# Optimization experiments

Hardware: AMD Instinct MI355X
Metric: run time of the kernel (lower is better)

The kernel has to match this reference:

```python
import jax, jax.numpy as jnp
import numpy as np

NUM_POINTS = 33  # must be 2n+1
N_T = 4_194_304  # number of time samples


def setup_inputs() -> dict:
    key = jax.random.key(0)
    k1, k2 = jax.random.split(key)
    x = jax.random.uniform(k1, (N_T,), dtype=jnp.float32)  # t in [0,1]
    P = jax.random.uniform(k2, (NUM_POINTS, 5), dtype=jnp.float32)
    P = (P - P.mean()) / P.std()  # mimics initLayers normalization
    return {"x": x, "P": P}


def _basis(d):
    """d: (N,1) -> quadratic Bezier basis (N,3) = [1, d, d^2] @ B."""
    B = jnp.array([[1., 0., 0.], [-2., 2., 0.], [1., -2., 1.]], dtype=d.dtype)
    tpow = jnp.concatenate([jnp.ones_like(d), d, d * d], axis=1)  # (N,3)
    return tpow @ B


def _forward(x, P):
    num_points = P.shape[0]
    S = num_points - 2  # num_splines
    p = P[:, :2]   # (num_points, 2) means
    s = P[:, 2:]   # (num_points, 3) packed symmetric 2x2: [a, b, c] -> [[a,b],[b,c]]
    # new_sigma_mat = sigma_mat^T @ sigma_mat (sigma_mat symmetric) packed back to 3 entries
    a, b, c = s[:, 0], s[:, 1], s[:, 2]
    sig = jnp.stack([a * a + b * b, b * (a + c), b * b + c * c], axis=1)  # (num_points, 3)

    t = x[:, None]                       # (N,1)
    N = x.shape[0]
    mu0 = jnp.zeros((N, 2), x.dtype)
    sg0 = jnp.zeros((N, 3), x.dtype)
    Pn0 = p[:3]                          # (3,2)
    Sn0 = sig[:3]                        # (3,3)
    ivals = jnp.arange(S - 1, dtype=x.dtype)
    Sm1 = jnp.asarray(S - 1, x.dtype)

    def step(carry, xs):
        Pn, Sn, mu, sg = carry
        i, p_next, s_next = xs
        d = (t * Sm1 - i) * 0.5                      # (N,1)
        choice = ((d >= 0) & (d <= 0.5)).astype(x.dtype)
        cw = jnp.cos(jnp.pi * d) ** 2
        sw = jnp.sin(jnp.pi * d) ** 2
        # mean control-point recurrence
        p0 = (Pn[0] + Pn[2]) / 4 + Pn[1] / 2
        p2 = p_next
        p1 = 2.0 * (Pn[2] - (p0 + p2) / 4)
        Pn2 = jnp.stack([p0, p1, p2])                # (3,2)
        f_prev = _basis(d + 0.5) @ Pn                # (N,2)
        f_curr = _basis(d) @ Pn2
        mu = (1 - choice) * mu + choice * (cw * f_prev + sw * f_curr)
        # variance control-point recurrence
        s0 = (Sn[0] + Sn[2]) / 16 + Sn[1] / 4
        s2 = s_next
        s1 = 4.0 * (Sn[2] - (s0 + s2) / 16)
        Sn2 = jnp.stack([s0, s1, s2])                # (3,3)
        g_prev = (_basis(d + 0.5) ** 2) @ Sn         # (N,3)
        g_curr = (_basis(d) ** 2) @ Sn2
        sg = (1 - choice) * sg + choice * (cw ** 2 * g_prev + sw ** 2 * g_curr)
        return (Pn2, Sn2, mu, sg), None

    (_, _, mu, sg), _ = jax.lax.scan(step, (Pn0, Sn0, mu0, sg0), (ivals, p[3:], sig[3:]))
    return mu, sg


def reference(x, P):
    return _forward(x, P)
```

## Files before the change

kernel.cpp:

```cpp
#include <hip/hip_runtime.h>
#include <math.h>

#define NENT 33
#define NQ   30
#define PPT  4
#define NBLK 2048

__device__ __forceinline__ unsigned short f2bf(float f) {
    unsigned int b = __float_as_uint(f);
    unsigned int r = (b + 0x7FFFu + ((b >> 16) & 1u)) >> 16;
    return (unsigned short)r;
}
__device__ __forceinline__ float bflo(unsigned int w) { return __uint_as_float(w << 16); }
__device__ __forceinline__ float bfhi(unsigned int w) { return __uint_as_float(w & 0xFFFF0000u); }

__global__ __launch_bounds__(256) void yuksel_fused(
    const float* __restrict__ x, const float* __restrict__ P,
    float* __restrict__ out, int N)
{
    __shared__ float stage[5][NENT];
    __shared__ uint2 qtab[5][NQ];
    const int tid = threadIdx.x;

    if (tid < NENT) {
        const int e = tid;
        float vals[5];
        if (e == 1) {
            float r0[5], r1[5], r2[5];
            for (int r = 0; r < 3; ++r) {
                float* dst = r==0 ? r0 : (r==1 ? r1 : r2);
                float a = P[r*5+2], b = P[r*5+3], c = P[r*5+4];
                dst[0] = P[r*5+0]; dst[1] = P[r*5+1];
                dst[2] = a*a + b*b; dst[3] = b*(a+c); dst[4] = b*b + c*c;
            }
            for (int k = 0; k < 2; ++k) vals[k] = (r0[k]+r2[k])*0.25f   + r1[k]*0.5f;
            for (int k = 2; k < 5; ++k) vals[k] = (r0[k]+r2[k])*0.0625f + r1[k]*0.25f;
        } else {
            float a = P[e*5+2], b = P[e*5+3], c = P[e*5+4];
            vals[0] = P[e*5+0]; vals[1] = P[e*5+1];
            vals[2] = a*a + b*b; vals[3] = b*(a+c); vals[4] = b*b + c*c;
        }
#pragma unroll
        for (int k = 0; k < 5; ++k) stage[k][e] = vals[k];
    }
    __syncthreads();

    if (tid < 5*NQ) {
        const int k = tid / NQ, e = tid % NQ;
        unsigned int h0 = f2bf(stage[k][e+0]), h1 = f2bf(stage[k][e+1]);
        unsigned int h2 = f2bf(stage[k][e+2]), h3 = f2bf(stage[k][e+3]);
        qtab[k][e] = make_uint2(h0 | (h1 << 16), h2 | (h3 << 16));
    }
    __syncthreads();

    const long long stride = (long long)gridDim.x * 256 * PPT;
    for (long long j0 = ((long long)blockIdx.x * 256 + tid) * PPT; j0 < N; j0 += stride) {
        float4 xv = *reinterpret_cast<const float4*>(x + j0);
        float xs[PPT] = { xv.x, xv.y, xv.z, xv.w };
        float mu[2*PPT], sg[3*PPT];

#pragma unroll
        for (int q = 0; q < PPT; ++q) {
            float u  = xs[q] * 30.0f;
            float fi = fminf(fmaxf(floorf(u), 0.0f), 29.0f);
            int   i  = (int)fi;
            float d  = (u - fi) * 0.5f;

            float cw  = 0.5f + 0.5f*__builtin_amdgcn_cosf(d);
            float sw  = 1.0f - cw;
            float cw2 = cw*cw, sw2 = sw*sw;

            float omd  = 1.0f - d;
            float om2d = 1.0f - 2.0f*d;
            float g    = d * om2d;
            float w0 = -cw * g;
            float w3 = -sw * g;
            float w1 = cw*(1.0f - 4.0f*d*d) + sw*omd*om2d;
            float w2 = cw*d*(1.0f + 2.0f*d) + 4.0f*sw*d*omd;

            float hp = 0.5f + d;
            float q14 = 1.0f - 4.0f*d*d;
            float v0 = -cw2 * g * (0.5f - d);
            float v3 = -sw2 * g * d;
            float v1 = cw2*q14*q14 + sw2*omd*omd*om2d;
            float v2 = cw2*2.0f*d*hp*hp + 16.0f*sw2*d*d*omd*omd;

            uint2 rpx = qtab[0][i];
            uint2 rpy = qtab[1][i];
            uint2 rs0 = qtab[2][i];
            uint2 rs1 = qtab[3][i];
            uint2 rs2 = qtab[4][i];

            mu[2*q+0] = w0*bflo(rpx.x) + w1*bfhi(rpx.x) + w2*bflo(rpx.y) + w3*bfhi(rpx.y);
            mu[2*q+1] = w0*bflo(rpy.x) + w1*bfhi(rpy.x) + w2*bflo(rpy.y) + w3*bfhi(rpy.y);
            sg[3*q+0] = v0*bflo(rs0.x) + v1*bfhi(rs0.x) + v2*bflo(rs0.y) + v3*bfhi(rs0.y);
            sg[3*q+1] = v0*bflo(rs1.x) + v1*bfhi(rs1.x) + v2*bflo(rs1.y) + v3*bfhi(rs1.y);
            sg[3*q+2] = v0*bflo(rs2.x) + v1*bfhi(rs2.x) + v2*bflo(rs2.y) + v3*bfhi(rs2.y);
        }

        float4* muOut = reinterpret_cast<float4*>(out + 2*j0);
        muOut[0] = make_float4(mu[0], mu[1], mu[2], mu[3]);
        muOut[1] = make_float4(mu[4], mu[5], mu[6], mu[7]);
        float4* sgOut = reinterpret_cast<float4*>(out + (size_t)2*N + 3*j0);
        sgOut[0] = make_float4(sg[0], sg[1], sg[2],  sg[3]);
        sgOut[1] = make_float4(sg[4], sg[5], sg[6],  sg[7]);
        sgOut[2] = make_float4(sg[8], sg[9], sg[10], sg[11]);
    }
}

extern "C" void kernel_launch(void* const* d_in, const int* in_sizes, int n_in,
                              void* d_out, int out_size, void* d_ws, size_t ws_size,
                              hipStream_t stream) {
    const float* x = (const float*)d_in[0];
    const float* P = (const float*)d_in[1];
    float* out = (float*)d_out;
    int N = in_sizes[0];

    const int threads = 256;
    const int per_block = threads * PPT;
    long long ntiles = (N + per_block - 1) / per_block;
    int blocks = (int)(ntiles < NBLK ? ntiles : NBLK);
    yuksel_fused<<<blocks, threads, 0, stream>>>(x, P, out, N);
}
```

Before: 26.38 us.

## Restructure per-wave chunking with LDS-staged coalesced sigma output stores

Each wave now processes a contiguous 256-element chunk, with every lane handling strided points. Loads and mu stores become lane-contiguous float2 writes, and the 3-wide sigma outputs are staged through LDS and written back as contiguous float4 stores. The intent is to replace the previous per-thread strided float4 writes with fully coalesced wave-wide stores. In exchange it adds LDS traffic, only a sched_barrier rather than a real wave-level sync around the LDS exchange, and a scalar tail path.

```diff
diff --git a/kernel.cpp b/kernel.cpp
--- a/kernel.cpp
+++ b/kernel.cpp
@@ -3,8 +3,9 @@
 
 #define NENT 33
 #define NQ   30
-#define PPT  4
 #define NBLK 2048
+#define WPB  4
+#define CHUNK 256
 
 __device__ __forceinline__ unsigned short f2bf(float f) {
     unsigned int b = __float_as_uint(f);
@@ -20,7 +21,10 @@
 {
     __shared__ float stage[5][NENT];
     __shared__ uint2 qtab[5][NQ];
-    const int tid = threadIdx.x;
+    __shared__ float sgbuf[WPB][3*CHUNK];
+    const int tid  = threadIdx.x;
+    const int lane = tid & 63;
+    const int wave = tid >> 6;
 
     if (tid < NENT) {
         const int e = tid;
@@ -53,14 +57,22 @@
     }
     __syncthreads();
 
-    const long long stride = (long long)gridDim.x * 256 * PPT;
-    for (long long j0 = ((long long)blockIdx.x * 256 + tid) * PPT; j0 < N; j0 += stride) {
-        float4 xv = *reinterpret_cast<const float4*>(x + j0);
-        float xs[PPT] = { xv.x, xv.y, xv.z, xv.w };
-        float mu[2*PPT], sg[3*PPT];
+    const int gwave = blockIdx.x * WPB + wave;
+    const long long chunk_stride = (long long)gridDim.x * WPB * CHUNK;
 
+    for (long long base = (long long)gwave * CHUNK; base < N; base += chunk_stride) {
+        const bool full = (base + CHUNK <= N);
+
+        float xs[4];
 #pragma unroll
-        for (int q = 0; q < PPT; ++q) {
+        for (int q = 0; q < 4; ++q) {
+            long long p = base + q*64 + lane;
+            xs[q] = (full || p < N) ? x[p] : 0.0f;
+        }
+
+        float m0[4], m1[4], sv0[4], sv1[4], sv2[4];
+#pragma unroll
+        for (int q = 0; q < 4; ++q) {
             float u  = xs[q] * 30.0f;
             float fi = fminf(fmaxf(floorf(u), 0.0f), 29.0f);
             int   i  = (int)fi;
@@ -78,7 +90,7 @@
             float w1 = cw*(1.0f - 4.0f*d*d) + sw*omd*om2d;
             float w2 = cw*d*(1.0f + 2.0f*d) + 4.0f*sw*d*omd;
 
-            float hp = 0.5f + d;
+            float hp  = 0.5f + d;
             float q14 = 1.0f - 4.0f*d*d;
             float v0 = -cw2 * g * (0.5f - d);
             float v3 = -sw2 * g * d;
@@ -91,20 +103,42 @@
             uint2 rs1 = qtab[3][i];
             uint2 rs2 = qtab[4][i];
 
-            mu[2*q+0] = w0*bflo(rpx.x) + w1*bfhi(rpx.x) + w2*bflo(rpx.y) + w3*bfhi(rpx.y);
-            mu[2*q+1] = w0*bflo(rpy.x) + w1*bfhi(rpy.x) + w2*bflo(rpy.y) + w3*bfhi(rpy.y);
-            sg[3*q+0] = v0*bflo(rs0.x) + v1*bfhi(rs0.x) + v2*bflo(rs0.y) + v3*bfhi(rs0.y);
-            sg[3*q+1] = v0*bflo(rs1.x) + v1*bfhi(rs1.x) + v2*bflo(rs1.y) + v3*bfhi(rs1.y);
-            sg[3*q+2] = v0*bflo(rs2.x) + v1*bfhi(rs2.x) + v2*bflo(rs2.y) + v3*bfhi(rs2.y);
+            m0[q]  = w0*bflo(rpx.x) + w1*bfhi(rpx.x) + w2*bflo(rpx.y) + w3*bfhi(rpx.y);
+            m1[q]  = w0*bflo(rpy.x) + w1*bfhi(rpy.x) + w2*bflo(rpy.y) + w3*bfhi(rpy.y);
+            sv0[q] = v0*bflo(rs0.x) + v1*bfhi(rs0.x) + v2*bflo(rs0.y) + v3*bfhi(rs0.y);
+            sv1[q] = v0*bflo(rs1.x) + v1*bfhi(rs1.x) + v2*bflo(rs1.y) + v3*bfhi(rs1.y);
+            sv2[q] = v0*bflo(rs2.x) + v1*bfhi(rs2.x) + v2*bflo(rs2.y) + v3*bfhi(rs2.y);
         }
 
-        float4* muOut = reinterpret_cast<float4*>(out + 2*j0);
-        muOut[0] = make_float4(mu[0], mu[1], mu[2], mu[3]);
-        muOut[1] = make_float4(mu[4], mu[5], mu[6], mu[7]);
-        float4* sgOut = reinterpret_cast<float4*>(out + (size_t)2*N + 3*j0);
-        sgOut[0] = make_float4(sg[0], sg[1], sg[2],  sg[3]);
-        sgOut[1] = make_float4(sg[4], sg[5], sg[6],  sg[7]);
-        sgOut[2] = make_float4(sg[8], sg[9], sg[10], sg[11]);
+        if (full) {
+#pragma unroll
+            for (int q = 0; q < 4; ++q) {
+                float2 v = make_float2(m0[q], m1[q]);
+                *reinterpret_cast<float2*>(out + 2*(base + q*64) + 2*lane) = v;
+            }
+#pragma unroll
+            for (int q = 0; q < 4; ++q) {
+                float* sb = &sgbuf[wave][(q*64 + lane)*3];
+                sb[0] = sv0[q]; sb[1] = sv1[q]; sb[2] = sv2[q];
+            }
+            __builtin_amdgcn_sched_barrier(0);
+            float* sgOutBase = out + (size_t)2*N + 3*base;
+#pragma unroll
+            for (int k = 0; k < 3; ++k) {
+                float4 v = *reinterpret_cast<const float4*>(&sgbuf[wave][k*256 + lane*4]);
+                *reinterpret_cast<float4*>(sgOutBase + k*256 + lane*4) = v;
+            }
+        } else {
+#pragma unroll
+            for (int q = 0; q < 4; ++q) {
+                long long p = base + q*64 + lane;
+                if (p < N) {
+                    out[2*p+0] = m0[q]; out[2*p+1] = m1[q];
+                    float* so = out + (size_t)2*N + 3*p;
+                    so[0] = sv0[q]; so[1] = sv1[q]; so[2] = sv2[q];
+                }
+            }
+        }
     }
 }
 
@@ -117,8 +151,8 @@
     int N = in_sizes[0];
 
     const int threads = 256;
-    const int per_block = threads * PPT;
-    long long ntiles = (N + per_block - 1) / per_block;
+    const int per_block = threads * 4;
+    long long ntiles = ((long long)N + per_block - 1) / per_block;
     int blocks = (int)(ntiles < NBLK ? ntiles : NBLK);
     yuksel_fused<<<blocks, threads, 0, stream>>>(x, P, out, N);
 }
```

Result: faster. 25.12 us (-4.8%).
